# Performance work log

Measured on AMD Instinct MI355X. Metric: run time of the kernel, lower is better.

Reference implementation:

```python
import jax, jax.numpy as jnp
import numpy as np

B, N, D, H, HD = 4, 2048, 512, 8, 64
FF = 1024
C2, HF, WF = 128, 64, 64
EPS = 1e-6


def setup_inputs() -> dict:
    key = jax.random.key(0)
    ks = jax.random.split(key, 9)
    def nrm(k, shape, s=0.02):
        return jax.random.normal(k, shape, dtype=jnp.float32) * s
    x = jax.random.normal(ks[0], (B, N, D), dtype=jnp.float32)
    theta = jax.random.normal(ks[1], (B, H, N, HD // 2), dtype=jnp.float32)
    fmaps = jax.random.normal(ks[2], (B, C2, HF, WF), dtype=jnp.float32)
    # pixel-unit (x, y) coords in [0, W-1] / [0, H-1]
    coords = jax.random.uniform(ks[3], (B, N, 2), dtype=jnp.float32) * (WF - 1)
    return dict(
        x=x, theta=theta, fmaps=fmaps, coords=coords,
        w_corr=nrm(ks[4], (D, C2)),
        norm1_scale=jnp.ones((D,), jnp.float32),
        qk_scale_q=jnp.ones((HD,), jnp.float32),
        qk_scale_k=jnp.ones((HD,), jnp.float32),
        w_qkv=nrm(ks[5], (3 * D, D)),
        w_out=nrm(ks[6], (D, D)),
        norm2_scale=jnp.ones((D,), jnp.float32),
        w_ff1=nrm(ks[7], (2 * FF, D)),
        b_ff1=jnp.zeros((2 * FF,), jnp.float32),
        w_ff2=nrm(ks[8], (D, FF)),
    )


def rms_norm(x, scale, eps=EPS):
    ms = jnp.mean(jnp.square(x), axis=-1, keepdims=True)
    return x * (scale * jax.lax.rsqrt(ms + eps))


def apply_rotary(x, theta):
    # rotates first 2*d channels of the head dim, as in _apply_rotary_emb_inplace
    d = theta.shape[-1]
    x1, x2 = x[..., :d], x[..., d:2 * d]
    cos, sin = jnp.cos(theta), jnp.sin(theta)
    y1 = x1 * cos - x2 * sin
    y2 = x2 * cos + x1 * sin
    return jnp.concatenate([y1, y2, x[..., 2 * d:]], axis=-1)


def bilinear_sample(fmaps, coords):
    # fmaps [B,C,H,W], coords [B,N,2] (x,y) pixels; border padding, align_corners=True
    Hh, Ww = fmaps.shape[-2], fmaps.shape[-1]
    xc = jnp.clip(coords[..., 0], 0.0, Ww - 1.0)
    yc = jnp.clip(coords[..., 1], 0.0, Hh - 1.0)
    x0 = jnp.floor(xc); y0 = jnp.floor(yc)
    wx = xc - x0; wy = yc - y0
    x0i = x0.astype(jnp.int32); x1i = jnp.minimum(x0i + 1, Ww - 1)
    y0i = y0.astype(jnp.int32); y1i = jnp.minimum(y0i + 1, Hh - 1)
    def gather_one(img, yi, xi):  # img [C,H,W] -> [C,N]
        return img[:, yi, xi]
    g = jax.vmap(gather_one)
    f00 = g(fmaps, y0i, x0i); f01 = g(fmaps, y0i, x1i)
    f10 = g(fmaps, y1i, x0i); f11 = g(fmaps, y1i, x1i)
    wx = wx[:, None, :]; wy = wy[:, None, :]
    top = f00 * (1.0 - wx) + f01 * wx
    bot = f10 * (1.0 - wx) + f11 * wx
    out = top * (1.0 - wy) + bot * wy  # [B,C,N]
    return jnp.transpose(out, (0, 2, 1))  # [B,N,C]


def reference(x, theta, fmaps, coords, w_corr, norm1_scale, qk_scale_q,
              qk_scale_k, w_qkv, w_out, norm2_scale, w_ff1, b_ff1, w_ff2):
    # correlation features injected into tokens
    feats = bilinear_sample(fmaps, coords)          # [B,N,C2]
    x = x + feats @ w_corr.T                        # [B,N,D]
    # --- attention block (pre-RMSNorm, qk-norm, RoPE, unscaled dot-product attn) ---
    skip = x
    xn = rms_norm(x, norm1_scale)
    qkv = xn @ w_qkv.T                              # [B,N,3D]
    q, k, v = jnp.split(qkv, 3, axis=-1)
    def to_heads(t):
        return jnp.transpose(t.reshape(t.shape[0], t.shape[1], H, HD), (0, 2, 1, 3))
    q, k, v = to_heads(q), to_heads(k), to_heads(v)  # [B,H,N,HD]
    q = rms_norm(q, qk_scale_q)
    k = rms_norm(k, qk_scale_k)
    q = apply_rotary(q, theta)
    k = apply_rotary(k, theta)
    # dot_product_attn: raw q @ k^T (no 1/sqrt(d)), softmax, @ v
    attn = jax.nn.softmax(jnp.einsum('bhid,bhjd->bhij', q, k), axis=-1)
    o = jnp.einsum('bhij,bhjd->bhid', attn, v)
    o = jnp.transpose(o, (0, 2, 1, 3)).reshape(x.shape[0], x.shape[1], D)
    x = skip + o @ w_out.T
    # --- feedforward block (GEGLU) ---
    skip = x
    xn = rms_norm(x, norm2_scale)
    h = xn @ w_ff1.T + b_ff1
    hx, gate = jnp.split(h, 2, axis=-1)
    h = hx * jax.nn.gelu(gate, approximate=False)
    return skip + h @ w_ff2.T
```

## Files before the change

### kernel.cpp

```cpp
#include <hip/hip_runtime.h>
#include <hip/hip_bf16.h>
#include <math.h>

#define Bsz 4
#define Nseq 2048
#define Dm 512
#define Hn 8
#define HDm 64
#define FFm 1024
#define Cc 128
#define EPSf 1e-6f

typedef __attribute__((ext_vector_type(8))) short short8;
typedef __attribute__((ext_vector_type(4))) float f32x4;
typedef __attribute__((ext_vector_type(16))) float f32x16;
typedef __attribute__((ext_vector_type(4))) unsigned u32x4;

#define AS1(p) ((__attribute__((address_space(1))) void*)((void*)(p)))
#define AS3(p) ((__attribute__((address_space(3))) void*)(p))

__device__ __forceinline__ float bf2f(unsigned short u) {
    return __uint_as_float(((unsigned)u) << 16);
}
__device__ __forceinline__ unsigned short f2bf(float f) {
    unsigned u = __float_as_uint(f);
    return (unsigned short)((u + 0x7fffu + ((u >> 16) & 1u)) >> 16);
}
__device__ __forceinline__ unsigned cvt_pk_bf16(float lo, float hi) {
    unsigned r;
    asm("v_cvt_pk_bf16_f32 %0, %1, %2" : "=v"(r) : "v"(lo), "v"(hi));
    return r;
}
__device__ __forceinline__ bool is_f32(const unsigned* dtp) {
    return dtp[0] == 0x3F800000u;
}

#define LOG2E 1.4426950408889634f
#define SHIFT2 92.33248261689366f

#define CONV_TOTAL 2690176
__global__ __launch_bounds__(256) void convert_kernel(
    const void* s0, const void* s1, const void* s2, const void* s3,
    const void* s4, const void* s5, const void* s6, const void* s7,
    const void* s8, const void* s9,
    unsigned short* __restrict__ canon, const unsigned* __restrict__ dtp)
{
    int i = blockIdx.x * 256 + threadIdx.x;
    if (i >= CONV_TOTAL) return;
    const void* src; int j;
    if      (i < 786432)  { src = s0; j = i; }
    else if (i < 1835008) {
        src = s1;
        int j0 = i - 786432;
        int rr = j0 >> 9, cc = j0 & 511;
        int q = rr >> 4, tt = rr & 15;
        j = ((q & 1) * 1024 + (q >> 1) * 16 + tt) * 512 + cc;
    }
    else if (i < 2359296) { src = s2; j = i - 1835008; }
    else if (i < 2621440) { src = s3; j = i - 2359296; }
    else if (i < 2686976) { src = s4; j = i - 2621440; }
    else if (i < 2689024) {
        src = s5;
        int j0 = i - 2686976;
        int q = j0 >> 4, tt = j0 & 15;
        j = (q & 1) * 1024 + (q >> 1) * 16 + tt;
    }
    else if (i < 2689536) { src = s6; j = i - 2689024; }
    else if (i < 2690048) { src = s7; j = i - 2689536; }
    else if (i < 2690112) { src = s8; j = i - 2690048; }
    else                  { src = s9; j = i - 2690112; }
    canon[i] = is_f32(dtp) ? f2bf(((const float*)src)[j])
                           : ((const unsigned short*)src)[j];
}

__global__ __launch_bounds__(256) void sample_kernel(
    const void* __restrict__ fmaps,
    const void* __restrict__ coords,
    unsigned short* __restrict__ feats,
    const unsigned* __restrict__ dtp)
{
    const bool f32m = is_f32(dtp);
    int i = blockIdx.x * 256 + threadIdx.x;
    int t = i >> 7;
    int c = i & 127;
    int b = t >> 11;
    float xc, yc;
    if (f32m) { xc = ((const float*)coords)[2 * t];  yc = ((const float*)coords)[2 * t + 1]; }
    else      { xc = bf2f(((const unsigned short*)coords)[2 * t]);
                yc = bf2f(((const unsigned short*)coords)[2 * t + 1]); }
    xc = fminf(fmaxf(xc, 0.f), 63.f);
    yc = fminf(fmaxf(yc, 0.f), 63.f);
    float x0f = floorf(xc), y0f = floorf(yc);
    float wx = xc - x0f, wy = yc - y0f;
    int x0 = (int)x0f, y0 = (int)y0f;
    int x1 = min(x0 + 1, 63), y1 = min(y0 + 1, 63);
    size_t fb = ((size_t)b * Cc + c) << 12;
    float f00, f01, f10, f11;
    if (f32m) {
        const float* fp = (const float*)fmaps + fb;
        f00 = fp[(y0 << 6) + x0]; f01 = fp[(y0 << 6) + x1];
        f10 = fp[(y1 << 6) + x0]; f11 = fp[(y1 << 6) + x1];
    } else {
        const unsigned short* fp = (const unsigned short*)fmaps + fb;
        f00 = bf2f(fp[(y0 << 6) + x0]); f01 = bf2f(fp[(y0 << 6) + x1]);
        f10 = bf2f(fp[(y1 << 6) + x0]); f11 = bf2f(fp[(y1 << 6) + x1]);
    }
    float top = f00 * (1.f - wx) + f01 * wx;
    float bot = f10 * (1.f - wx) + f11 * wx;
    feats[i] = f2bf(top * (1.f - wy) + bot * wy);
}

template<int BN>
__global__ __launch_bounds__(256, 4) void gemm_bt(
    const unsigned short* __restrict__ A,
    const unsigned short* __restrict__ W,
    const unsigned short* __restrict__ bias,
    const float* __restrict__ resF,
    const void* __restrict__ resRaw,
    float* __restrict__ outF,
    unsigned short* __restrict__ outB,
    void* __restrict__ outRaw,
    unsigned short* __restrict__ outG,
    const unsigned* __restrict__ dtp,
    int M, int N, int K)
{
    constexpr int NT = BN / 32;
    __shared__ __align__(16) unsigned short As[2][128 * 32];
    __shared__ __align__(16) unsigned short Bs[2][BN * 32];
    const int tid = threadIdx.x;
    const int wave = tid >> 6, lane = tid & 63;
    const int quad = lane >> 4, l16 = lane & 15;
    const int wm = wave >> 1, wn = wave & 1;
    const int rowBase = blockIdx.y * 128;
    const int colBase = blockIdx.x * BN;
    const unsigned short* Ab = A + (size_t)rowBase * K;
    const unsigned short* Wb = W + (size_t)colBase * K;
    const int sr = lane >> 2;
    const int sc = (lane & 3) * 8;

    f32x4 acc[4][NT] = {};

    auto stage = [&](int buf, int k0) {
#pragma unroll
        for (int c = 0; c < 2; ++c) {
            int chunk = wave + c * 4;
            const unsigned short* ga = Ab + (size_t)(chunk * 16 + sr) * K + k0 + sc;
            __builtin_amdgcn_global_load_lds(AS1(ga), AS3(&As[buf][chunk * 512]), 16, 0, 0);
        }
#pragma unroll
        for (int c = 0; c < BN / 16; c += 4) {
            int chunk = wave + c;
            const unsigned short* gb = Wb + (size_t)(chunk * 16 + sr) * K + k0 + sc;
            __builtin_amdgcn_global_load_lds(AS1(gb), AS3(&Bs[buf][chunk * 512]), 16, 0, 0);
        }
    };

    const int nk = K >> 5;
    stage(0, 0);
    for (int kt = 0; kt < nk; ++kt) {
        const int buf = kt & 1;
        __syncthreads();
        __builtin_amdgcn_sched_barrier(0);
        if (kt + 1 < nk) stage(1 - buf, (kt + 1) << 5);
        short8 af[4], bfr[NT];
#pragma unroll
        for (int mt = 0; mt < 4; ++mt)
            af[mt] = *(const short8*)&As[buf][(wm * 64 + mt * 16 + l16) * 32 + quad * 8];
#pragma unroll
        for (int nt = 0; nt < NT; ++nt)
            bfr[nt] = *(const short8*)&Bs[buf][(wn * (BN / 2) + nt * 16 + l16) * 32 + quad * 8];
        __builtin_amdgcn_s_setprio(1);
#pragma unroll
        for (int mt = 0; mt < 4; ++mt)
#pragma unroll
            for (int nt = 0; nt < NT; ++nt)
                acc[mt][nt] = __builtin_amdgcn_mfma_f32_16x16x32_bf16(
                    af[mt], bfr[nt], acc[mt][nt], 0, 0, 0);
        __builtin_amdgcn_s_setprio(0);
    }

    if (outG) {
#pragma unroll
        for (int mt = 0; mt < 4; ++mt)
#pragma unroll
            for (int r = 0; r < 4; ++r) {
                int row = rowBase + wm * 64 + mt * 16 + quad * 4 + r;
#pragma unroll
                for (int nt = 0; nt < NT; nt += 2) {
                    int colh = colBase + wn * (BN / 2) + nt * 16 + l16;
                    float hx = acc[mt][nt][r]     + bf2f(bias[colh]);
                    float g  = acc[mt][nt + 1][r] + bf2f(bias[colh + 16]);
                    float gl = 0.5f * g * (1.f + erff(g * 0.70710678118654752f));
                    int pc = (colBase >> 1) + wn * (BN / 4) + (nt >> 1) * 16 + l16;
                    outG[(size_t)row * FFm + pc] = f2bf(hx * gl);
                }
            }
        return;
    }
    const bool f32m = dtp ? is_f32(dtp) : false;
#pragma unroll
    for (int mt = 0; mt < 4; ++mt) {
#pragma unroll
        for (int r = 0; r < 4; ++r) {
            int row = rowBase + wm * 64 + mt * 16 + quad * 4 + r;
            size_t rowoff = (size_t)row * N;
#pragma unroll
            for (int nt = 0; nt < NT; ++nt) {
                int col = colBase + wn * (BN / 2) + nt * 16 + l16;
                float v = acc[mt][nt][r];
                if (bias) v += bf2f(bias[col]);
                size_t idx = rowoff + col;
                if (resF) v += resF[idx];
                if (resRaw) v += f32m ? ((const float*)resRaw)[idx]
                                      : bf2f(((const unsigned short*)resRaw)[idx]);
                if (outF)      outF[idx] = v;
                else if (outB) outB[idx] = f2bf(v);
                else if (f32m) ((float*)outRaw)[idx] = v;
                else           ((unsigned short*)outRaw)[idx] = f2bf(v);
            }
        }
    }
}

__global__ __launch_bounds__(256) void rmsnorm_kernel(
    const float* __restrict__ X, const unsigned short* __restrict__ scale,
    unsigned short* __restrict__ Y)
{
    int t = blockIdx.x;
    int tid = threadIdx.x;
    const float* xr = X + (size_t)t * 512;
    float a = xr[tid], b = xr[tid + 256];
    float ss = a * a + b * b;
#pragma unroll
    for (int off = 1; off < 64; off <<= 1) ss += __shfl_xor(ss, off);
    __shared__ float red[4];
    int wave = tid >> 6, lane = tid & 63;
    if (lane == 0) red[wave] = ss;
    __syncthreads();
    float tot = red[0] + red[1] + red[2] + red[3];
    float r = rsqrtf(tot * (1.f / 512.f) + EPSf);
    Y[(size_t)t * 512 + tid]       = f2bf(a * (bf2f(scale[tid]) * r));
    Y[(size_t)t * 512 + tid + 256] = f2bf(b * (bf2f(scale[tid + 256]) * r));
}

__global__ __launch_bounds__(256) void qkv_rope_kernel(
    const unsigned short* __restrict__ qkv, const void* __restrict__ theta,
    const unsigned short* __restrict__ sq, const unsigned short* __restrict__ sk,
    unsigned short* __restrict__ Qo, unsigned short* __restrict__ Ko,
    const unsigned* __restrict__ dtp)
{
    const bool f32m = is_f32(dtp);
    int t = blockIdx.x;
    int b = t >> 11, n = t & 2047;
    int wave = threadIdx.x >> 6, lane = threadIdx.x & 63;
    const unsigned short* base = qkv + (size_t)t * 1536;
#pragma unroll
    for (int hh = 0; hh < 2; ++hh) {
        int h = wave + hh * 4;
        float q = bf2f(base[h * 64 + lane]);
        float k = bf2f(base[512 + h * 64 + lane]);
        float ssq = q * q, ssk = k * k;
#pragma unroll
        for (int off = 1; off < 64; off <<= 1) {
            ssq += __shfl_xor(ssq, off);
            ssk += __shfl_xor(ssk, off);
        }
        float qn = q * (bf2f(sq[lane]) * rsqrtf(ssq * (1.f / 64.f) + EPSf));
        float kn = k * (bf2f(sk[lane]) * rsqrtf(ssk * (1.f / 64.f) + EPSf));
        size_t thIdx = ((size_t)(b * Hn + h) * Nseq + n) * 32 + (lane & 31);
        float th = f32m ? ((const float*)theta)[thIdx]
                        : bf2f(((const unsigned short*)theta)[thIdx]);
        float cth = __cosf(th), sth = __sinf(th);
        float qp = __shfl_xor(qn, 32);
        float kp = __shfl_xor(kn, 32);
        float sgn = (lane < 32) ? -1.f : 1.f;
        float qr = qn * cth + sgn * qp * sth;
        float kr = kn * cth + sgn * kp * sth;
        size_t o = ((size_t)(b * Hn + h) * Nseq + n) * 64 + lane;
        Qo[o] = f2bf(qr * LOG2E);
        int ktn = n >> 6, rhn = (n >> 5) & 1, l31n = n & 31;
        int kcd = lane >> 4, hhd = (lane >> 3) & 1, jd = lane & 7;
        size_t koff = (((((size_t)(b * Hn + h) * 32 + ktn) * 4 + kcd) * 2 + rhn) * 64
                       + hhd * 32 + l31n) * 8 + jd;
        Ko[koff] = f2bf(kr);
    }
}

__global__ __launch_bounds__(256) void vtrans_kernel(
    const unsigned short* __restrict__ qkvb, unsigned short* __restrict__ Vt)
{
    int bh = blockIdx.y;
    int b = bh >> 3, h = bh & 7;
    int tid = threadIdx.x;
    int d = tid & 63;
    int chunk = blockIdx.x * 4 + (tid >> 6);
    int n0 = chunk * 8;
    unsigned short v[8];
#pragma unroll
    for (int j = 0; j < 8; ++j)
        v[j] = qkvb[((size_t)(b * Nseq + n0 + j)) * 1536 + 1024 + h * 64 + d];
    int ktn = n0 >> 6, kcn = (n0 >> 4) & 3, hhn = (n0 >> 3) & 1;
    int rhd = d >> 5, l31d = d & 31;
    size_t voff = (((((size_t)bh * 32 + ktn) * 4 + kcn) * 2 + rhd) * 64
                   + hhn * 32 + l31d) * 8;
    *(short8*)&Vt[voff] = *(short8*)v;
}

__global__ __launch_bounds__(256, 4) void attn_kernel(
    const unsigned short* __restrict__ Qg,
    const unsigned short* __restrict__ Kf,
    const unsigned short* __restrict__ Vf,
    float* __restrict__ Op,
    float* __restrict__ Lp)
{
    const int bh = blockIdx.x;
    const int b = bh >> 3, h = bh & 7;
    const int q0 = blockIdx.y * 128;
    const int kz = blockIdx.z;
    const int tid = threadIdx.x;
    const int wave = tid >> 6, lane = tid & 63;
    const int l31 = lane & 31, hh = lane >> 5;
    const size_t bhN = (size_t)bh * Nseq;
    const bool hi = (hh == 1);

    short8 bq[4];
#pragma unroll
    for (int kc = 0; kc < 4; ++kc)
        bq[kc] = *(const short8*)&Qg[(bhN + q0 + wave * 32 + l31) * 64 + kc * 16 + hh * 8];

    f32x16 oa[2] = {};
    float lsum = 0.f;

    const unsigned short* kfb = Kf + (size_t)bh * (32 * 4096) + (size_t)lane * 8;
    const unsigned short* vfb = Vf + (size_t)bh * (32 * 4096) + (size_t)lane * 8;

    const int KT0 = kz * (Nseq / 128);
    const int KT1 = KT0 + (Nseq / 128);

    for (int kt = KT0; kt < KT1; ++kt) {
        const unsigned short* kp = kfb + (size_t)kt * 4096;
        const unsigned short* vp = vfb + (size_t)kt * 4096;

        short8 kf0[4], kf1[4];
#pragma unroll
        for (int kc = 0; kc < 4; ++kc) {
            kf0[kc] = *(const short8*)(kp + kc * 1024);
            kf1[kc] = *(const short8*)(kp + kc * 1024 + 512);
        }

        f32x16 st[2];
#pragma unroll
        for (int mt = 0; mt < 2; ++mt)
#pragma unroll
            for (int e = 0; e < 16; ++e) st[mt][e] = -SHIFT2;
        __builtin_amdgcn_s_setprio(1);
#pragma unroll
        for (int kc = 0; kc < 4; ++kc) {
            st[0] = __builtin_amdgcn_mfma_f32_32x32x16_bf16(kf0[kc], bq[kc], st[0], 0, 0, 0);
            st[1] = __builtin_amdgcn_mfma_f32_32x32x16_bf16(kf1[kc], bq[kc], st[1], 0, 0, 0);
        }
        __builtin_amdgcn_s_setprio(0);
        __builtin_amdgcn_sched_barrier(0);

        short8 vf0[4], vf1[4];
#pragma unroll
        for (int kc = 0; kc < 4; ++kc) {
            vf0[kc] = *(const short8*)(vp + kc * 1024);
            vf1[kc] = *(const short8*)(vp + kc * 1024 + 512);
        }

        unsigned pk[2][8];
        float partial = 0.f;
#pragma unroll
        for (int t = 0; t < 2; ++t)
#pragma unroll
            for (int p = 0; p < 4; ++p) {
                float v0 = __builtin_amdgcn_exp2f(st[t][4 * p + 0]);
                float v1 = __builtin_amdgcn_exp2f(st[t][4 * p + 1]);
                float v2 = __builtin_amdgcn_exp2f(st[t][4 * p + 2]);
                float v3 = __builtin_amdgcn_exp2f(st[t][4 * p + 3]);
                partial += (v0 + v1) + (v2 + v3);
                pk[t][2 * p + 0] = cvt_pk_bf16(v0, v1);
                pk[t][2 * p + 1] = cvt_pk_bf16(v2, v3);
            }
        lsum += partial + __shfl_xor(partial, 32);

        __builtin_amdgcn_s_setprio(1);
#pragma unroll
        for (int kc = 0; kc < 4; ++kc) {
            const int tau = kc >> 1;
            const int pA = 2 * (kc & 1);
            const int pB = pA + 1;
            unsigned dA0 = pk[tau][2 * pA], dA1 = pk[tau][2 * pA + 1];
            unsigned dB0 = pk[tau][2 * pB], dB1 = pk[tau][2 * pB + 1];
            unsigned s0 = hi ? dA0 : dB0, s1 = hi ? dA1 : dB1;
            unsigned r0 = __shfl_xor(s0, 32), r1 = __shfl_xor(s1, 32);
            unsigned o0 = hi ? dB0 : dA0, o1 = hi ? dB1 : dA1;
            u32x4 av = { hi ? r0 : o0, hi ? r1 : o1,
                         hi ? o0 : r0, hi ? o1 : r1 };
            short8 ap = __builtin_bit_cast(short8, av);
            oa[0] = __builtin_amdgcn_mfma_f32_32x32x16_bf16(ap, vf0[kc], oa[0], 0, 0, 0);
            oa[1] = __builtin_amdgcn_mfma_f32_32x32x16_bf16(ap, vf1[kc], oa[1], 0, 0, 0);
        }
        __builtin_amdgcn_s_setprio(0);
    }

    if (!hi)
        Lp[((size_t)kz * 32 + bh) * Nseq + q0 + wave * 32 + l31] = lsum;
    const size_t obase = (size_t)kz * (Bsz * Nseq);
#pragma unroll
    for (int nt = 0; nt < 2; ++nt)
#pragma unroll
        for (int i = 0; i < 16; ++i) {
            int qr = q0 + wave * 32 + (i & 3) + 8 * (i >> 2) + 4 * hh;
            Op[(obase + (size_t)b * Nseq + qr) * Dm + h * 64 + nt * 32 + l31] =
                oa[nt][i];
        }
}

__global__ __launch_bounds__(256) void attn_combine_kernel(
    const float* __restrict__ Op,
    const float* __restrict__ Lp,
    unsigned short* __restrict__ Og)
{
    int gid = blockIdx.x * 256 + threadIdx.x;
    size_t base = (size_t)gid * 8;
    int t = gid >> 6;
    int c = (gid & 63) * 8;
    int h = c >> 6;
    int bh = ((t >> 11) << 3) + h;
    int n = t & 2047;
    float l = Lp[(size_t)bh * Nseq + n] + Lp[(size_t)(32 * Nseq) + (size_t)bh * Nseq + n];
    float inv = 1.f / l;
    f32x4 a0 = *(const f32x4*)&Op[base];
    f32x4 a1 = *(const f32x4*)&Op[base + 4];
    f32x4 b0 = *(const f32x4*)&Op[(size_t)8192 * 512 + base];
    f32x4 b1 = *(const f32x4*)&Op[(size_t)8192 * 512 + base + 4];
    unsigned short o[8];
#pragma unroll
    for (int j = 0; j < 4; ++j) {
        o[j]     = f2bf((a0[j] + b0[j]) * inv);
        o[4 + j] = f2bf((a1[j] + b1[j]) * inv);
    }
    *(short8*)&Og[base] = *(short8*)o;
}

extern "C" void kernel_launch(void* const* d_in, const int* in_sizes, int n_in,
                              void* d_out, int out_size, void* d_ws, size_t ws_size,
                              hipStream_t stream) {
    const void* x      = d_in[0];
    const void* theta  = d_in[1];
    const void* fmaps  = d_in[2];
    const void* coords = d_in[3];
    const void* w_corr = d_in[4];
    const void* n1s    = d_in[5];
    const void* sq     = d_in[6];
    const void* sk     = d_in[7];
    const void* w_qkv  = d_in[8];
    const void* w_out  = d_in[9];
    const void* n2s    = d_in[10];
    const void* w_ff1  = d_in[11];
    const void* b_ff1  = d_in[12];
    const void* w_ff2  = d_in[13];
    const unsigned* dtp = (const unsigned*)n1s;

    char* ws = (char*)d_ws;
    float*          x1    = (float*)(ws + 0);
    float*          x2    = (float*)(ws + 16777216);
    unsigned short* xn    = (unsigned short*)(ws + 33554432);
    unsigned short* qkvb  = (unsigned short*)(ws + 41943040);
    unsigned short* feats = (unsigned short*)(ws + 41943040);
    unsigned short* qb    = (unsigned short*)(ws + 67108864);
    unsigned short* kb    = (unsigned short*)(ws + 75497472);
    unsigned short* vt    = (unsigned short*)(ws + 83886080);
    unsigned short* ob    = (unsigned short*)(ws + 92274688);
    unsigned short* hbuf  = (unsigned short*)(ws + 75497472);
    unsigned short* canon = (unsigned short*)(ws + 100663296);
    float*          opart = (float*)(ws + 16777216);
    float*          lpart = (float*)(ws + 50331648);
    unsigned short* wqkvc  = canon + 0;
    unsigned short* wff1c  = canon + 786432;
    unsigned short* wff2c  = canon + 1835008;
    unsigned short* woutc  = canon + 2359296;
    unsigned short* wcorrc = canon + 2621440;
    unsigned short* bff1c  = canon + 2686976;
    unsigned short* n1c    = canon + 2689024;
    unsigned short* n2c    = canon + 2689536;
    unsigned short* sqc    = canon + 2690048;
    unsigned short* skc    = canon + 2690112;

    convert_kernel<<<(CONV_TOTAL + 255) / 256, 256, 0, stream>>>(
        w_qkv, w_ff1, w_ff2, w_out, w_corr, b_ff1, n1s, n2s, sq, sk, canon, dtp);
    sample_kernel<<<4096, 256, 0, stream>>>(fmaps, coords, feats, dtp);
    gemm_bt<64><<<dim3(8, 64), 256, 0, stream>>>(feats, wcorrc, nullptr, nullptr, x,
                                                 x1, nullptr, nullptr, nullptr, dtp, 8192, 512, 128);
    rmsnorm_kernel<<<8192, 256, 0, stream>>>(x1, n1c, xn);
    gemm_bt<128><<<dim3(12, 64), 256, 0, stream>>>(xn, wqkvc, nullptr, nullptr, nullptr,
                                                   nullptr, qkvb, nullptr, nullptr, nullptr, 8192, 1536, 512);
    qkv_rope_kernel<<<8192, 256, 0, stream>>>(qkvb, theta, sqc, skc, qb, kb, dtp);
    vtrans_kernel<<<dim3(64, 32), 256, 0, stream>>>(qkvb, vt);
    attn_kernel<<<dim3(32, 16, 2), 256, 0, stream>>>(qb, kb, vt, opart, lpart);
    attn_combine_kernel<<<2048, 256, 0, stream>>>(opart, lpart, ob);
    gemm_bt<64><<<dim3(8, 64), 256, 0, stream>>>(ob, woutc, nullptr, x1, nullptr,
                                                 x2, nullptr, nullptr, nullptr, nullptr, 8192, 512, 512);
    rmsnorm_kernel<<<8192, 256, 0, stream>>>(x2, n2c, xn);
    gemm_bt<128><<<dim3(16, 64), 256, 0, stream>>>(xn, wff1c, bff1c, nullptr, nullptr,
                                                   nullptr, nullptr, nullptr, hbuf, nullptr, 8192, 2048, 512);
    gemm_bt<64><<<dim3(8, 64), 256, 0, stream>>>(hbuf, wff2c, nullptr, x2, nullptr,
                                                 nullptr, nullptr, d_out, nullptr, dtp, 8192, 512, 1024);
}
```

Baseline: 385.9 us.

## Stage K/V tiles into LDS with double-buffered async global_load_lds

```diff
diff --git a/kernel.cpp b/kernel.cpp
--- a/kernel.cpp
+++ b/kernel.cpp
@@ -320,8 +320,9 @@
     const int tid = threadIdx.x;
     const int wave = tid >> 6, lane = tid & 63;
     const int l31 = lane & 31, hh = lane >> 5;
+    const bool hi = (hh == 1);
     const size_t bhN = (size_t)bh * Nseq;
-    const bool hi = (hh == 1);
+    __shared__ __align__(16) unsigned short KVs[2][8192];
 
     short8 bq[4];
 #pragma unroll
@@ -331,21 +332,40 @@
     f32x16 oa[2] = {};
     float lsum = 0.f;
 
-    const unsigned short* kfb = Kf + (size_t)bh * (32 * 4096) + (size_t)lane * 8;
-    const unsigned short* vfb = Vf + (size_t)bh * (32 * 4096) + (size_t)lane * 8;
+    const unsigned short* kgb = Kf + (size_t)bh * (32 * 4096) + (size_t)lane * 8;
+    const unsigned short* vgb = Vf + (size_t)bh * (32 * 4096) + (size_t)lane * 8;
+
+    auto stage = [&](int buf, int kt) {
+        const unsigned short* kg = kgb + (size_t)kt * 4096;
+        const unsigned short* vg = vgb + (size_t)kt * 4096;
+#pragma unroll
+        for (int c = 0; c < 2; ++c) {
+            int cc = wave + c * 4;
+            __builtin_amdgcn_global_load_lds(AS1(kg + cc * 512),
+                                             AS3(&KVs[buf][cc * 512]), 16, 0, 0);
+            __builtin_amdgcn_global_load_lds(AS1(vg + cc * 512),
+                                             AS3(&KVs[buf][4096 + cc * 512]), 16, 0, 0);
+        }
+    };
 
     const int KT0 = kz * (Nseq / 128);
     const int KT1 = KT0 + (Nseq / 128);
 
+    stage(0, KT0);
     for (int kt = KT0; kt < KT1; ++kt) {
-        const unsigned short* kp = kfb + (size_t)kt * 4096;
-        const unsigned short* vp = vfb + (size_t)kt * 4096;
+        const int cur = (kt - KT0) & 1;
+        __syncthreads();
+        __builtin_amdgcn_sched_barrier(0);
+        if (kt + 1 < KT1) stage(cur ^ 1, kt + 1);
+
+        const unsigned short* kb_ = &KVs[cur][lane * 8];
+        const unsigned short* vb_ = &KVs[cur][4096 + lane * 8];
 
         short8 kf0[4], kf1[4];
 #pragma unroll
         for (int kc = 0; kc < 4; ++kc) {
-            kf0[kc] = *(const short8*)(kp + kc * 1024);
-            kf1[kc] = *(const short8*)(kp + kc * 1024 + 512);
+            kf0[kc] = *(const short8*)(kb_ + kc * 1024);
+            kf1[kc] = *(const short8*)(kb_ + kc * 1024 + 512);
         }
 
         f32x16 st[2];
@@ -360,14 +380,6 @@
             st[1] = __builtin_amdgcn_mfma_f32_32x32x16_bf16(kf1[kc], bq[kc], st[1], 0, 0, 0);
         }
         __builtin_amdgcn_s_setprio(0);
-        __builtin_amdgcn_sched_barrier(0);
-
-        short8 vf0[4], vf1[4];
-#pragma unroll
-        for (int kc = 0; kc < 4; ++kc) {
-            vf0[kc] = *(const short8*)(vp + kc * 1024);
-            vf1[kc] = *(const short8*)(vp + kc * 1024 + 512);
-        }
 
         unsigned pk[2][8];
         float partial = 0.f;
@@ -399,8 +411,10 @@
             u32x4 av = { hi ? r0 : o0, hi ? r1 : o1,
                          hi ? o0 : r0, hi ? o1 : r1 };
             short8 ap = __builtin_bit_cast(short8, av);
-            oa[0] = __builtin_amdgcn_mfma_f32_32x32x16_bf16(ap, vf0[kc], oa[0], 0, 0, 0);
-            oa[1] = __builtin_amdgcn_mfma_f32_32x32x16_bf16(ap, vf1[kc], oa[1], 0, 0, 0);
+            short8 bv0 = *(const short8*)(vb_ + kc * 1024);
+            short8 bv1 = *(const short8*)(vb_ + kc * 1024 + 512);
+            oa[0] = __builtin_amdgcn_mfma_f32_32x32x16_bf16(ap, bv0, oa[0], 0, 0, 0);
+            oa[1] = __builtin_amdgcn_mfma_f32_32x32x16_bf16(ap, bv1, oa[1], 0, 0, 0);
         }
         __builtin_amdgcn_s_setprio(0);
     }
```

Measured after the change: 354.3 us. 1.09x faster.
